# Optimization experiments

Measured on AMD Instinct MI355X. Metric: run time of the kernel, lower is better.

Reference implementation:

```python
import jax, jax.numpy as jnp
import numpy as np

N, E, B = 50000, 800000, 1000
NODE_DIN, BB_DOUT, DHID, K = 32, 64, 64, 3
GLOB_DIN, EMBED_DIN = 64, 64
CIN = BB_DOUT + NODE_DIN  # 96


def setup_inputs() -> dict:
    key = jax.random.key(0)
    ks = jax.random.split(key, 24)

    def w(k, shape, fan_in):
        return jax.random.normal(k, shape, jnp.float32) / np.float32(np.sqrt(fan_in))

    inp = dict(
        x=jax.random.normal(ks[0], (N, NODE_DIN), jnp.float32),
        u=jax.random.normal(ks[1], (B, GLOB_DIN), jnp.float32),
        z=jax.random.normal(ks[2], (N, BB_DOUT), jnp.float32),
        edge_index=jax.random.randint(ks[3], (2, E), 0, N),
        edge_weight=jax.random.uniform(ks[4], (E,), jnp.float32),
        batch=jnp.sort(jax.random.randint(ks[5], (N,), 0, B)),
        batch_size=B,
        prev_h=jax.random.normal(ks[6], (N, DHID), jnp.float32),
    )
    # six ChebConvs of GConvGRU: x-convs take CIN, h-convs take DHID; all output DHID
    for i, nm in enumerate(["xz", "hz", "xr", "hr", "xh", "hh"]):
        cin = CIN if nm[0] == "x" else DHID
        inp[f"W{nm}"] = w(ks[7 + 2 * i], (K, cin, DHID), cin * K)
        inp[f"b{nm}"] = jnp.zeros((DHID,), jnp.float32)
    inp["Wg"] = w(ks[20], (GLOB_DIN, EMBED_DIN), GLOB_DIN)
    inp["bg"] = jnp.zeros((EMBED_DIN,), jnp.float32)
    return inp


def _cheb(xin, W, b, src, dst, w_norm, n):
    """ChebConv with sym norm, lambda_max=2 -> L_hat = -D^-1/2 A D^-1/2 (diag cancels)."""
    def prop(t):  # L_hat @ t  ([N,C])
        return -jax.ops.segment_sum(w_norm[:, None] * t[src], dst, num_segments=n)

    out = xin @ W[0] + b
    tx_prev = xin
    tx = None
    if W.shape[0] > 1:
        tx = prop(xin)
        out = out + tx @ W[1]
    for k in range(2, W.shape[0]):
        tx_new = 2.0 * prop(tx) - tx_prev
        out = out + tx_new @ W[k]
        tx_prev, tx = tx, tx_new
    return out


def reference(x, u, z, edge_index, edge_weight, batch, batch_size, prev_h,
              Wxz, bxz, Whz, bhz, Wxr, bxr, Whr, bhr, Wxh, bxh, Whh, bhh, Wg, bg):
    n = x.shape[0]
    src, dst = edge_index[0], edge_index[1]
    deg = jax.ops.segment_sum(edge_weight, src, num_segments=n)
    deg_safe = jnp.where(deg > 0, deg, 1.0)
    dinv = jnp.where(deg > 0, jax.lax.rsqrt(deg_safe), 0.0)
    w_norm = dinv[src] * edge_weight * dinv[dst]

    xin = jnp.concatenate([z, x], axis=-1)  # [N, CIN]
    Z = jax.nn.sigmoid(_cheb(xin, Wxz, bxz, src, dst, w_norm, n)
                       + _cheb(prev_h, Whz, bhz, src, dst, w_norm, n))
    R = jax.nn.sigmoid(_cheb(xin, Wxr, bxr, src, dst, w_norm, n)
                       + _cheb(prev_h, Whr, bhr, src, dst, w_norm, n))
    Ht = jnp.tanh(_cheb(xin, Wxh, bxh, src, dst, w_norm, n)
                  + _cheb(prev_h * R, Whh, bhh, src, dst, w_norm, n))
    h = Z * prev_h + (1.0 - Z) * Ht

    graph_emb = jax.ops.segment_sum(z, batch, num_segments=batch_size)  # [B, BB_DOUT]
    global_emb = jax.nn.relu(u @ Wg + bg)                                # [B, EMBED_DIN]
    fused = jnp.concatenate([graph_emb, global_emb], axis=-1)           # [B, 128]
    return fused, h
```

## Files before the change

kernel.cpp:

```cpp
#include <hip/hip_runtime.h>

#define NN 50000
#define EE 800000
#define BB 1000
#define NB 196

typedef unsigned short u16;
typedef __attribute__((ext_vector_type(8))) short bf16x8;
typedef __attribute__((ext_vector_type(4))) float f32x4;

static __device__ __forceinline__ u16 f2b(float f) {
    union { float f; unsigned u; } v;
    v.f = f;
    unsigned r = v.u + 0x7fffu + ((v.u >> 16) & 1u);
    return (u16)(r >> 16);
}

static __device__ __forceinline__ float b2f(short s) {
    union { unsigned u; float f; } c;
    c.u = ((unsigned)(u16)s) << 16;
    return c.f;
}

__global__ void k_degcnt(const int* __restrict__ src, const int* __restrict__ dst,
                         const float* __restrict__ ew, float* __restrict__ deg,
                         int* __restrict__ cnt) {
    int e = blockIdx.x * 256 + threadIdx.x;
    if (e >= EE) return;
    atomicAdd(&deg[src[e]], ew[e]);
    atomicAdd(&cnt[dst[e]], 1);
}

__global__ void k_scan1(const int* __restrict__ cnt, int* __restrict__ incl,
                        int* __restrict__ bsum) {
    __shared__ int s[256];
    int i = blockIdx.x * 256 + threadIdx.x;
    int v = (i < NN) ? cnt[i] : 0;
    s[threadIdx.x] = v;
    __syncthreads();
    for (int off = 1; off < 256; off <<= 1) {
        int t = (threadIdx.x >= off) ? s[threadIdx.x - off] : 0;
        __syncthreads();
        s[threadIdx.x] += t;
        __syncthreads();
    }
    if (i < NN) incl[i] = s[threadIdx.x];
    if (threadIdx.x == 255) bsum[blockIdx.x] = s[255];
}

__global__ void k_scan2(int* __restrict__ bsum) {
    __shared__ int s[256];
    int v = (threadIdx.x < NB) ? bsum[threadIdx.x] : 0;
    s[threadIdx.x] = v;
    __syncthreads();
    for (int off = 1; off < 256; off <<= 1) {
        int t = (threadIdx.x >= off) ? s[threadIdx.x - off] : 0;
        __syncthreads();
        s[threadIdx.x] += t;
        __syncthreads();
    }
    if (threadIdx.x < NB) bsum[threadIdx.x] = s[threadIdx.x];
}

__global__ void k_scan3(const int* __restrict__ incl, const int* __restrict__ cnt,
                        const int* __restrict__ bsum, int* __restrict__ row_ptr,
                        int* __restrict__ cursor, float* __restrict__ deg) {
    int i = blockIdx.x * 256 + threadIdx.x;
    if (i >= NN) return;
    int off = (blockIdx.x > 0) ? bsum[blockIdx.x - 1] : 0;
    int start = off + incl[i] - cnt[i];
    row_ptr[i] = start;
    cursor[i] = start;
    float d = deg[i];
    deg[i] = d > 0.f ? rsqrtf(d) : 0.f;
}

__global__ void k_scatter(const int* __restrict__ src, const int* __restrict__ dst,
                          const float* __restrict__ ew, const float* __restrict__ dinv,
                          int* __restrict__ cursor, uint2* __restrict__ csr8) {
    int e = blockIdx.x * 256 + threadIdx.x;
    if (e >= EE) return;
    int d = dst[e], s = src[e];
    int pos = atomicAdd(&cursor[d], 1);
    float w = dinv[s] * ew[e] * dinv[d];
    csr8[pos] = make_uint2((unsigned)s, __float_as_uint(w));
}

__global__ void k_build_A(const float* __restrict__ z, const float* __restrict__ x,
                          const float* __restrict__ ph, u16* __restrict__ A) {
    int i = blockIdx.x * 256 + threadIdx.x;
    if (i >= NN * 160) return;
    int n = i / 160, c = i - n * 160;
    float v;
    int ofs;
    if (c < 64) {
        v = z[n * 64 + c];
        ofs = c;
    } else if (c < 96) {
        v = x[n * 32 + (c - 64)];
        ofs = c;
    } else {
        v = ph[n * 64 + (c - 96)];
        ofs = 288 + (c - 96);
    }
    A[(size_t)n * 480 + ofs] = f2b(v);
}

__global__ void k_packW_all(const float* __restrict__ Wxz, const float* __restrict__ Wxr,
                            const float* __restrict__ Wxh, const float* __restrict__ Whz,
                            const float* __restrict__ Whr, const float* __restrict__ Whh,
                            u16* __restrict__ Wp, u16* __restrict__ W3p) {
    int idx = blockIdx.x * 256 + threadIdx.x;
    if (idx < 15 * 12 * 512) {
        int j = idx & 7, l = (idx >> 3) & 63;
        int ct = (idx >> 9) % 12, s = (idx >> 9) / 12;
        int k = 32 * s + (l >> 4) * 8 + j;
        int g = ct >> 2;
        int c = 16 * (ct & 3) + (l & 15);
        float val;
        if (k < 288) {
            int ki = k / 96, kr = k - ki * 96;
            const float* W = (g == 0) ? Wxz : ((g == 1) ? Wxr : Wxh);
            val = W[(ki * 96 + kr) * 64 + c];
        } else if (g == 2) {
            val = 0.f;
        } else {
            int km = k - 288;
            int ki = km >> 6, kr = km & 63;
            const float* W = (g == 0) ? Whz : Whr;
            val = W[(ki * 64 + kr) * 64 + c];
        }
        Wp[idx] = f2b(val);
    } else {
        int i2 = idx - 15 * 12 * 512;
        if (i2 >= 6 * 4 * 512) return;
        int j = i2 & 7, l = (i2 >> 3) & 63;
        int ct = (i2 >> 9) & 3, s = i2 >> 11;
        int k = 32 * s + (l >> 4) * 8 + j;
        int ki = k >> 6, kr = k & 63;
        int c = 16 * ct + (l & 15);
        W3p[i2] = f2b(Whh[(ki * 64 + kr) * 64 + c]);
    }
}

template <int C, int SCALE, bool HB, int BS, int OS>
__global__ __launch_bounds__(BS) void k_pull(
    const u16* __restrict__ Abase, int inofs, int baseofs, int outofs,
    const uint2* __restrict__ csr8, const int* __restrict__ row_ptr,
    const int* __restrict__ cnt) {
    constexpr int TPR = C / 8;
    int tid = blockIdx.x * BS + threadIdx.x;
    int r = tid / TPR;
    int c8 = (tid - r * TPR) * 8;
    if (r >= NN) return;
    int s0 = row_ptr[r], n = cnt[r];
    float acc[8] = {0.f, 0.f, 0.f, 0.f, 0.f, 0.f, 0.f, 0.f};
    const u16* in = Abase + inofs + c8;
    uint2 e = (n > 0) ? csr8[s0] : make_uint2(0u, 0u);
    for (int j = 0; j < n; j++) {
        uint2 ec = e;
        if (j + 1 < n) e = csr8[s0 + j + 1];
        float w = __uint_as_float(ec.y);
        bf16x8 v = *(const bf16x8*)(in + (size_t)ec.x * OS);
#pragma unroll
        for (int k = 0; k < 8; k++) acc[k] += w * b2f(v[k]);
    }
    const float sc = -(float)SCALE;
    float o[8];
    if (HB) {
        bf16x8 b = *(const bf16x8*)(Abase + (size_t)r * OS + baseofs + c8);
#pragma unroll
        for (int k = 0; k < 8; k++) o[k] = sc * acc[k] - b2f(b[k]);
    } else {
#pragma unroll
        for (int k = 0; k < 8; k++) o[k] = sc * acc[k];
    }
    bf16x8 p;
#pragma unroll
    for (int k = 0; k < 8; k++) p[k] = (short)f2b(o[k]);
    *(bf16x8*)(const_cast<u16*>(Abase) + (size_t)r * OS + outofs + c8) = p;
}

__global__ __launch_bounds__(256) void k_gates_mfma(
    const u16* __restrict__ A, const u16* __restrict__ Wp,
    const float* __restrict__ bxz, const float* __restrict__ bhz,
    const float* __restrict__ bxr, const float* __restrict__ bhr,
    const float* __restrict__ bxh, const float* __restrict__ ph,
    float* __restrict__ Zb, float* __restrict__ Hx, u16* __restrict__ A3) {
    int wv = (blockIdx.x * 256 + threadIdx.x) >> 6;
    int lane = threadIdx.x & 63;
    int r0 = wv * 16;
    if (r0 >= NN) return;
    int q = lane >> 4, j0 = lane & 15;

    f32x4 acc[12];
#pragma unroll
    for (int i = 0; i < 12; i++) acc[i] = (f32x4){0.f, 0.f, 0.f, 0.f};

    const u16* arow = A + (size_t)(r0 + j0) * 480 + q * 8;
#pragma unroll
    for (int s = 0; s < 15; s++) {
        bf16x8 a = *(const bf16x8*)(arow + 32 * s);
        const u16* bp = Wp + (size_t)(s * 12) * 512 + lane * 8;
#pragma unroll
        for (int ct = 0; ct < 12; ct++) {
            bf16x8 b = *(const bf16x8*)(bp + ct * 512);
            acc[ct] = __builtin_amdgcn_mfma_f32_16x16x32_bf16(a, b, acc[ct], 0, 0, 0);
        }
    }

#pragma unroll
    for (int ct = 0; ct < 4; ct++) {
        int j = 16 * ct + j0;
        float bz = bxz[j] + bhz[j];
        float br = bxr[j] + bhr[j];
        float bh = bxh[j];
#pragma unroll
        for (int reg = 0; reg < 4; reg++) {
            int r = r0 + q * 4 + reg;
            size_t i = (size_t)r * 64 + j;
            float zp = acc[ct][reg] + bz;
            float rp = acc[ct + 4][reg] + br;
            float hp = acc[ct + 8][reg] + bh;
            float zv = 1.f / (1.f + expf(-zp));
            float rv = 1.f / (1.f + expf(-rp));
            float hv = rv * ph[i];
            Zb[i] = zv;
            Hx[i] = hp;
            A3[(size_t)r * 192 + j] = f2b(hv);
        }
    }
}

__global__ __launch_bounds__(256) void k_final_mfma(
    const u16* __restrict__ A3, const u16* __restrict__ W3p,
    const float* __restrict__ bhh, const float* __restrict__ Hx,
    const float* __restrict__ Zb, const float* __restrict__ ph,
    float* __restrict__ outh) {
    int wv = (blockIdx.x * 256 + threadIdx.x) >> 6;
    int lane = threadIdx.x & 63;
    int r0 = wv * 16;
    if (r0 >= NN) return;
    int q = lane >> 4, j0 = lane & 15;

    f32x4 acc[4];
#pragma unroll
    for (int i = 0; i < 4; i++) acc[i] = (f32x4){0.f, 0.f, 0.f, 0.f};

    const u16* arow = A3 + (size_t)(r0 + j0) * 192 + q * 8;
#pragma unroll
    for (int s = 0; s < 6; s++) {
        bf16x8 a = *(const bf16x8*)(arow + 32 * s);
        const u16* bp = W3p + (size_t)(s * 4) * 512 + lane * 8;
#pragma unroll
        for (int ct = 0; ct < 4; ct++) {
            bf16x8 b = *(const bf16x8*)(bp + ct * 512);
            acc[ct] = __builtin_amdgcn_mfma_f32_16x16x32_bf16(a, b, acc[ct], 0, 0, 0);
        }
    }

#pragma unroll
    for (int ct = 0; ct < 4; ct++) {
        int j = 16 * ct + j0;
        float bh = bhh[j];
#pragma unroll
        for (int reg = 0; reg < 4; reg++) {
            int r = r0 + q * 4 + reg;
            size_t i = (size_t)r * 64 + j;
            float ht = tanhf(Hx[i] + acc[ct][reg] + bh);
            float zv = Zb[i];
            outh[i] = zv * ph[i] + (1.f - zv) * ht;
        }
    }
}

__global__ void k_gemb(const float* __restrict__ z, const int* __restrict__ batch,
                       float* __restrict__ gemb) {
    int wave = (blockIdx.x * 256 + threadIdx.x) >> 6;
    int lane = threadIdx.x & 63;
    int n0 = wave * 64;
    if (n0 >= NN) return;
    int nend = n0 + 64 < NN ? n0 + 64 : NN;
    float acc = 0.f;
    int cur = batch[n0];
    for (int n = n0; n < nend; n++) {
        int b = batch[n];
        if (b != cur) {
            atomicAdd(&gemb[(size_t)cur * 64 + lane], acc);
            acc = 0.f;
            cur = b;
        }
        acc += z[(size_t)n * 64 + lane];
    }
    atomicAdd(&gemb[(size_t)cur * 64 + lane], acc);
}

__global__ __launch_bounds__(256) void k_fused(
    const float* __restrict__ u, const float* __restrict__ Wg, const float* __restrict__ bg,
    const float* __restrict__ gemb, float* __restrict__ out) {
    int t = blockIdx.x * 256 + threadIdx.x;
    int r = t >> 6, c = t & 63;
    if (r >= BB) return;
    float acc = bg[c];
    const float* ur = u + (size_t)r * 64;
    for (int k = 0; k < 64; k++) acc += ur[k] * Wg[k * 64 + c];
    acc = fmaxf(acc, 0.f);
    out[(size_t)r * 128 + c] = gemb[(size_t)r * 64 + c];
    out[(size_t)r * 128 + 64 + c] = acc;
}

extern "C" void kernel_launch(void* const* d_in, const int* in_sizes, int n_in,
                              void* d_out, int out_size, void* d_ws, size_t ws_size,
                              hipStream_t stream) {
    const float* x  = (const float*)d_in[0];
    const float* u  = (const float*)d_in[1];
    const float* z  = (const float*)d_in[2];
    const int*   ei = (const int*)d_in[3];
    const float* ew = (const float*)d_in[4];
    const int* batch = (const int*)d_in[5];
    const float* ph = (const float*)d_in[7];
    const float *Wxz = (const float*)d_in[8],  *bxz = (const float*)d_in[9];
    const float *Whz = (const float*)d_in[10], *bhz = (const float*)d_in[11];
    const float *Wxr = (const float*)d_in[12], *bxr = (const float*)d_in[13];
    const float *Whr = (const float*)d_in[14], *bhr = (const float*)d_in[15];
    const float *Wxh = (const float*)d_in[16], *bxh = (const float*)d_in[17];
    const float *Whh = (const float*)d_in[18], *bhh = (const float*)d_in[19];
    const float *Wg  = (const float*)d_in[20], *bg  = (const float*)d_in[21];
    const int* src = ei;
    const int* dst = ei + EE;

    char* wsb = (char*)d_ws;
    size_t o = 0;
    auto alloc = [&](size_t bytes) {
        void* p = wsb + o;
        o += (bytes + 255) & ~(size_t)255;
        return p;
    };
    int*   degcnt  = (int*)alloc(2 * NN * 4);
    float* deg     = (float*)degcnt;
    int*   cnt     = degcnt + NN;
    int*   incl    = (int*)alloc(NN * 4);
    int*   row_ptr = (int*)alloc(NN * 4);
    int*   cursor  = (int*)alloc(NN * 4);
    int*   bsum    = (int*)alloc(256 * 4);
    uint2* csr8    = (uint2*)alloc((size_t)EE * 8);
    float* Zb   = (float*)alloc((size_t)NN * 64 * 4);
    float* Hx   = (float*)alloc((size_t)NN * 64 * 4);
    float* gemb = (float*)alloc((size_t)BB * 64 * 4);
    u16*   A    = (u16*)alloc((size_t)NN * 480 * 2);
    u16*   A3   = (u16*)alloc((size_t)NN * 192 * 2);
    u16*   Wp   = (u16*)alloc(15 * 12 * 512 * 2);
    u16*   W3p  = (u16*)alloc(6 * 4 * 512 * 2);

    float* outF = (float*)d_out;
    float* outH = outF + (size_t)BB * 128;

    const int BLK = 256;
    const int gE = (EE + BLK - 1) / BLK;
    const int gA = (NN * 160 + BLK - 1) / BLK;
    const int gPull96 = (NN + 15) / 16;
    const int gPull64 = (NN + 31) / 32;
    const int gMFMA = (3125 + 3) / 4;
    const int gPack = (15 * 12 * 512 + 6 * 4 * 512 + BLK - 1) / BLK;

    hipMemsetAsync(degcnt, 0, 2 * NN * 4, stream);
    k_degcnt<<<gE, BLK, 0, stream>>>(src, dst, ew, deg, cnt);

    k_scan1<<<NB, 256, 0, stream>>>(cnt, incl, bsum);
    k_scan2<<<1, 256, 0, stream>>>(bsum);
    k_scan3<<<NB, 256, 0, stream>>>(incl, cnt, bsum, row_ptr, cursor, deg);
    k_scatter<<<gE, BLK, 0, stream>>>(src, dst, ew, deg, cursor, csr8);

    k_packW_all<<<gPack, BLK, 0, stream>>>(Wxz, Wxr, Wxh, Whz, Whr, Whh, Wp, W3p);
    k_build_A<<<gA, BLK, 0, stream>>>(z, x, ph, A);

    k_pull<96, 1, false, 192, 480><<<gPull96, 192, 0, stream>>>(A, 0, 0, 96, csr8, row_ptr, cnt);
    k_pull<96, 2, true, 192, 480><<<gPull96, 192, 0, stream>>>(A, 96, 0, 192, csr8, row_ptr, cnt);
    k_pull<64, 1, false, 256, 480><<<gPull64, 256, 0, stream>>>(A, 288, 0, 352, csr8, row_ptr, cnt);
    k_pull<64, 2, true, 256, 480><<<gPull64, 256, 0, stream>>>(A, 352, 288, 416, csr8, row_ptr, cnt);

    k_gates_mfma<<<gMFMA, BLK, 0, stream>>>(A, Wp, bxz, bhz, bxr, bhr, bxh, ph, Zb, Hx, A3);

    k_pull<64, 1, false, 256, 192><<<gPull64, 256, 0, stream>>>(A3, 0, 0, 64, csr8, row_ptr, cnt);
    k_pull<64, 2, true, 256, 192><<<gPull64, 256, 0, stream>>>(A3, 64, 0, 128, csr8, row_ptr, cnt);

    k_final_mfma<<<gMFMA, BLK, 0, stream>>>(A3, W3p, bhh, Hx, Zb, ph, outH);

    hipMemsetAsync(gemb, 0, (size_t)BB * 64 * 4, stream);
    k_gemb<<<(NN + BLK - 1) / BLK, BLK, 0, stream>>>(z, batch, gemb);
    k_fused<<<(BB * 64 + BLK - 1) / BLK, BLK, 0, stream>>>(u, Wg, bg, gemb, outF);
}
```

Before: 480.8 us.

## Interleave x/h features for merged 160-wide pulls, privatize degree atomics, bf16 intermediates

Rearranges the A buffer so the input features and prev_h sit next to each other (160 columns). The two Chebyshev propagation passes can then run as two 160-wide pulls instead of four separate 96- and 64-wide pulls, which cuts the number of passes over the edge list. Degree and count atomics are spread over 8 per-block copies to reduce atomic contention, and the copies are summed in the scan kernels. Zb and Hx are stored as bf16, and prev_h is read back from the bf16 A buffer instead of the fp32 input, which cuts traffic at some cost in precision.

```diff
diff --git a/kernel.cpp b/kernel.cpp
--- a/kernel.cpp
+++ b/kernel.cpp
@@ -4,6 +4,7 @@
 #define EE 800000
 #define BB 1000
 #define NB 196
+#define NCOPY 8
 
 typedef unsigned short u16;
 typedef __attribute__((ext_vector_type(8))) short bf16x8;
@@ -23,19 +24,25 @@
 }
 
 __global__ void k_degcnt(const int* __restrict__ src, const int* __restrict__ dst,
-                         const float* __restrict__ ew, float* __restrict__ deg,
-                         int* __restrict__ cnt) {
+                         const float* __restrict__ ew, float* __restrict__ deg_p,
+                         int* __restrict__ cnt_p) {
     int e = blockIdx.x * 256 + threadIdx.x;
     if (e >= EE) return;
-    atomicAdd(&deg[src[e]], ew[e]);
-    atomicAdd(&cnt[dst[e]], 1);
-}
-
-__global__ void k_scan1(const int* __restrict__ cnt, int* __restrict__ incl,
-                        int* __restrict__ bsum) {
+    int cp = blockIdx.x & (NCOPY - 1);
+    atomicAdd(&deg_p[(size_t)cp * NN + src[e]], ew[e]);
+    atomicAdd(&cnt_p[(size_t)cp * NN + dst[e]], 1);
+}
+
+__global__ void k_scan1(const int* __restrict__ cnt_p, int* __restrict__ cnt,
+                        int* __restrict__ incl, int* __restrict__ bsum) {
     __shared__ int s[256];
     int i = blockIdx.x * 256 + threadIdx.x;
-    int v = (i < NN) ? cnt[i] : 0;
+    int v = 0;
+    if (i < NN) {
+#pragma unroll
+        for (int p = 0; p < NCOPY; p++) v += cnt_p[(size_t)p * NN + i];
+        cnt[i] = v;
+    }
     s[threadIdx.x] = v;
     __syncthreads();
     for (int off = 1; off < 256; off <<= 1) {
@@ -64,15 +71,18 @@
 
 __global__ void k_scan3(const int* __restrict__ incl, const int* __restrict__ cnt,
                         const int* __restrict__ bsum, int* __restrict__ row_ptr,
-                        int* __restrict__ cursor, float* __restrict__ deg) {
+                        int* __restrict__ cursor, const float* __restrict__ deg_p,
+                        float* __restrict__ dinv) {
     int i = blockIdx.x * 256 + threadIdx.x;
     if (i >= NN) return;
     int off = (blockIdx.x > 0) ? bsum[blockIdx.x - 1] : 0;
     int start = off + incl[i] - cnt[i];
     row_ptr[i] = start;
     cursor[i] = start;
-    float d = deg[i];
-    deg[i] = d > 0.f ? rsqrtf(d) : 0.f;
+    float d = 0.f;
+#pragma unroll
+    for (int p = 0; p < NCOPY; p++) d += deg_p[(size_t)p * NN + i];
+    dinv[i] = d > 0.f ? rsqrtf(d) : 0.f;
 }
 
 __global__ void k_scatter(const int* __restrict__ src, const int* __restrict__ dst,
@@ -92,18 +102,10 @@
     if (i >= NN * 160) return;
     int n = i / 160, c = i - n * 160;
     float v;
-    int ofs;
-    if (c < 64) {
-        v = z[n * 64 + c];
-        ofs = c;
-    } else if (c < 96) {
-        v = x[n * 32 + (c - 64)];
-        ofs = c;
-    } else {
-        v = ph[n * 64 + (c - 96)];
-        ofs = 288 + (c - 96);
-    }
-    A[(size_t)n * 480 + ofs] = f2b(v);
+    if (c < 64) v = z[n * 64 + c];
+    else if (c < 96) v = x[n * 32 + (c - 64)];
+    else v = ph[n * 64 + (c - 96)];
+    A[(size_t)n * 480 + c] = f2b(v);
 }
 
 __global__ void k_packW_all(const float* __restrict__ Wxz, const float* __restrict__ Wxr,
@@ -117,18 +119,23 @@
         int k = 32 * s + (l >> 4) * 8 + j;
         int g = ct >> 2;
         int c = 16 * (ct & 3) + (l & 15);
+        bool isX;
+        int kr;
+        if (k < 96)       { isX = true;  kr = k; }
+        else if (k < 160) { isX = false; kr = k - 96; }
+        else if (k < 256) { isX = true;  kr = 96 + (k - 160); }
+        else if (k < 320) { isX = false; kr = 64 + (k - 256); }
+        else if (k < 416) { isX = true;  kr = 192 + (k - 320); }
+        else              { isX = false; kr = 128 + (k - 416); }
         float val;
-        if (k < 288) {
-            int ki = k / 96, kr = k - ki * 96;
+        if (isX) {
             const float* W = (g == 0) ? Wxz : ((g == 1) ? Wxr : Wxh);
-            val = W[(ki * 96 + kr) * 64 + c];
+            val = W[kr * 64 + c];
         } else if (g == 2) {
             val = 0.f;
         } else {
-            int km = k - 288;
-            int ki = km >> 6, kr = km & 63;
             const float* W = (g == 0) ? Whz : Whr;
-            val = W[(ki * 64 + kr) * 64 + c];
+            val = W[kr * 64 + c];
         }
         Wp[idx] = f2b(val);
     } else {
@@ -185,8 +192,8 @@
     const u16* __restrict__ A, const u16* __restrict__ Wp,
     const float* __restrict__ bxz, const float* __restrict__ bhz,
     const float* __restrict__ bxr, const float* __restrict__ bhr,
-    const float* __restrict__ bxh, const float* __restrict__ ph,
-    float* __restrict__ Zb, float* __restrict__ Hx, u16* __restrict__ A3) {
+    const float* __restrict__ bxh,
+    u16* __restrict__ Zb16, u16* __restrict__ Hx16, u16* __restrict__ A3) {
     int wv = (blockIdx.x * 256 + threadIdx.x) >> 6;
     int lane = threadIdx.x & 63;
     int r0 = wv * 16;
@@ -224,18 +231,18 @@
             float hp = acc[ct + 8][reg] + bh;
             float zv = 1.f / (1.f + expf(-zp));
             float rv = 1.f / (1.f + expf(-rp));
-            float hv = rv * ph[i];
-            Zb[i] = zv;
-            Hx[i] = hp;
-            A3[(size_t)r * 192 + j] = f2b(hv);
+            float phv = b2f((short)A[(size_t)r * 480 + 96 + j]);
+            Zb16[i] = f2b(zv);
+            Hx16[i] = f2b(hp);
+            A3[(size_t)r * 192 + j] = f2b(rv * phv);
         }
     }
 }
 
 __global__ __launch_bounds__(256) void k_final_mfma(
     const u16* __restrict__ A3, const u16* __restrict__ W3p,
-    const float* __restrict__ bhh, const float* __restrict__ Hx,
-    const float* __restrict__ Zb, const float* __restrict__ ph,
+    const float* __restrict__ bhh, const u16* __restrict__ Hx16,
+    const u16* __restrict__ Zb16, const u16* __restrict__ A,
     float* __restrict__ outh) {
     int wv = (blockIdx.x * 256 + threadIdx.x) >> 6;
     int lane = threadIdx.x & 63;
@@ -267,9 +274,10 @@
         for (int reg = 0; reg < 4; reg++) {
             int r = r0 + q * 4 + reg;
             size_t i = (size_t)r * 64 + j;
-            float ht = tanhf(Hx[i] + acc[ct][reg] + bh);
-            float zv = Zb[i];
-            outh[i] = zv * ph[i] + (1.f - zv) * ht;
+            float ht = tanhf(b2f((short)Hx16[i]) + acc[ct][reg] + bh);
+            float zv = b2f((short)Zb16[i]);
+            float phv = b2f((short)A[(size_t)r * 480 + 96 + j]);
+            outh[i] = zv * phv + (1.f - zv) * ht;
         }
     }
 }
@@ -336,16 +344,17 @@
         o += (bytes + 255) & ~(size_t)255;
         return p;
     };
-    int*   degcnt  = (int*)alloc(2 * NN * 4);
-    float* deg     = (float*)degcnt;
-    int*   cnt     = degcnt + NN;
+    float* deg_p   = (float*)alloc((size_t)NCOPY * NN * 4);
+    int*   cnt_p   = (int*)alloc((size_t)NCOPY * NN * 4);
+    int*   cnt     = (int*)alloc(NN * 4);
     int*   incl    = (int*)alloc(NN * 4);
     int*   row_ptr = (int*)alloc(NN * 4);
     int*   cursor  = (int*)alloc(NN * 4);
+    float* dinv    = (float*)alloc(NN * 4);
     int*   bsum    = (int*)alloc(256 * 4);
     uint2* csr8    = (uint2*)alloc((size_t)EE * 8);
-    float* Zb   = (float*)alloc((size_t)NN * 64 * 4);
-    float* Hx   = (float*)alloc((size_t)NN * 64 * 4);
+    u16*   Zb16 = (u16*)alloc((size_t)NN * 64 * 2);
+    u16*   Hx16 = (u16*)alloc((size_t)NN * 64 * 2);
     float* gemb = (float*)alloc((size_t)BB * 64 * 4);
     u16*   A    = (u16*)alloc((size_t)NN * 480 * 2);
     u16*   A3   = (u16*)alloc((size_t)NN * 192 * 2);
@@ -358,33 +367,31 @@
     const int BLK = 256;
     const int gE = (EE + BLK - 1) / BLK;
     const int gA = (NN * 160 + BLK - 1) / BLK;
-    const int gPull96 = (NN + 15) / 16;
+    const int gPull160 = (NN + 15) / 16;
     const int gPull64 = (NN + 31) / 32;
     const int gMFMA = (3125 + 3) / 4;
     const int gPack = (15 * 12 * 512 + 6 * 4 * 512 + BLK - 1) / BLK;
 
-    hipMemsetAsync(degcnt, 0, 2 * NN * 4, stream);
-    k_degcnt<<<gE, BLK, 0, stream>>>(src, dst, ew, deg, cnt);
-
-    k_scan1<<<NB, 256, 0, stream>>>(cnt, incl, bsum);
-    k_scan2<<<1, 256, 0, stream>>>(bsum);
-    k_scan3<<<NB, 256, 0, stream>>>(incl, cnt, bsum, row_ptr, cursor, deg);
-    k_scatter<<<gE, BLK, 0, stream>>>(src, dst, ew, deg, cursor, csr8);
-
     k_packW_all<<<gPack, BLK, 0, stream>>>(Wxz, Wxr, Wxh, Whz, Whr, Whh, Wp, W3p);
     k_build_A<<<gA, BLK, 0, stream>>>(z, x, ph, A);
 
-    k_pull<96, 1, false, 192, 480><<<gPull96, 192, 0, stream>>>(A, 0, 0, 96, csr8, row_ptr, cnt);
-    k_pull<96, 2, true, 192, 480><<<gPull96, 192, 0, stream>>>(A, 96, 0, 192, csr8, row_ptr, cnt);
-    k_pull<64, 1, false, 256, 480><<<gPull64, 256, 0, stream>>>(A, 288, 0, 352, csr8, row_ptr, cnt);
-    k_pull<64, 2, true, 256, 480><<<gPull64, 256, 0, stream>>>(A, 352, 288, 416, csr8, row_ptr, cnt);
-
-    k_gates_mfma<<<gMFMA, BLK, 0, stream>>>(A, Wp, bxz, bhz, bxr, bhr, bxh, ph, Zb, Hx, A3);
+    hipMemsetAsync(deg_p, 0, (size_t)2 * NCOPY * NN * 4, stream);
+    k_degcnt<<<gE, BLK, 0, stream>>>(src, dst, ew, deg_p, cnt_p);
+
+    k_scan1<<<NB, 256, 0, stream>>>(cnt_p, cnt, incl, bsum);
+    k_scan2<<<1, 256, 0, stream>>>(bsum);
+    k_scan3<<<NB, 256, 0, stream>>>(incl, cnt, bsum, row_ptr, cursor, deg_p, dinv);
+    k_scatter<<<gE, BLK, 0, stream>>>(src, dst, ew, dinv, cursor, csr8);
+
+    k_pull<160, 1, false, 320, 480><<<gPull160, 320, 0, stream>>>(A, 0, 0, 160, csr8, row_ptr, cnt);
+    k_pull<160, 2, true, 320, 480><<<gPull160, 320, 0, stream>>>(A, 160, 0, 320, csr8, row_ptr, cnt);
+
+    k_gates_mfma<<<gMFMA, BLK, 0, stream>>>(A, Wp, bxz, bhz, bxr, bhr, bxh, Zb16, Hx16, A3);
 
     k_pull<64, 1, false, 256, 192><<<gPull64, 256, 0, stream>>>(A3, 0, 0, 64, csr8, row_ptr, cnt);
     k_pull<64, 2, true, 256, 192><<<gPull64, 256, 0, stream>>>(A3, 64, 0, 128, csr8, row_ptr, cnt);
 
-    k_final_mfma<<<gMFMA, BLK, 0, stream>>>(A3, W3p, bhh, Hx, Zb, ph, outH);
+    k_final_mfma<<<gMFMA, BLK, 0, stream>>>(A3, W3p, bhh, Hx16, Zb16, A, outH);
 
     hipMemsetAsync(gemb, 0, (size_t)BB * 64 * 4, stream);
     k_gemb<<<(NN + BLK - 1) / BLK, BLK, 0, stream>>>(z, batch, gemb);
```

Result: faster. 455.5 us (-5.3%).
